# Optimization experiments

Measured on AMD Instinct MI355X. Metric: run time of the kernel, lower is better.

The kernel has to match this reference:

```python
import jax, jax.numpy as jnp
import numpy as np

DIM = 1024
H = 16
DH = 64
INNER = H * DH
SCALE = DH ** -0.5


def setup_inputs() -> dict:
    key = jax.random.key(0)
    ks = jax.random.split(key, 6)
    B, L, R = 4, 4096, 512
    x = jax.random.normal(ks[0], (B, L, DIM), dtype=jnp.float32)
    context = jax.random.normal(ks[1], (B, R, DIM), dtype=jnp.float32)
    s = DIM ** -0.5
    Wq = jax.random.normal(ks[2], (DIM, INNER), dtype=jnp.float32) * s
    Wk = jax.random.normal(ks[3], (DIM, INNER), dtype=jnp.float32) * s
    Wv = jax.random.normal(ks[4], (DIM, INNER), dtype=jnp.float32) * s
    Wo = jax.random.normal(ks[5], (INNER, DIM), dtype=jnp.float32) * (INNER ** -0.5)
    return {"x": x, "context": context, "Wq": Wq, "Wk": Wk, "Wv": Wv, "Wo": Wo}


def reference(x, context, Wq, Wk, Wv, Wo):
    B, L, _ = x.shape
    R = context.shape[1]
    # project and split heads: (B, H, L/R, Dh)
    q = (x @ Wq).reshape(B, L, H, DH).transpose(0, 2, 1, 3)
    k = (context @ Wk).reshape(B, R, H, DH).transpose(0, 2, 1, 3)
    v = (context @ Wv).reshape(B, R, H, DH).transpose(0, 2, 1, 3)
    scores = jnp.einsum('bhld,bhrd->bhlr', q, k) * SCALE  # (B,H,L,R)
    attn = jax.nn.softmax(scores, axis=-1)
    out = jnp.einsum('bhlr,bhrd->bhld', attn, v)
    out = out.transpose(0, 2, 1, 3).reshape(B, L, INNER)
    return out @ Wo
```

## Files before the change

### kernel.cpp

```cpp
#include <hip/hip_runtime.h>
#include <hip/hip_bf16.h>

#define DIMC 1024
#define HEADS 16
#define DHEAD 64
#define LQ 4096
#define RK 512
#define BATCH 4

#define QSCALE 0.18033688011112042f

using bf16x8  = __attribute__((ext_vector_type(8))) __bf16;
using short4v = __attribute__((ext_vector_type(4))) short;
using f32x4   = __attribute__((ext_vector_type(4))) float;

__device__ inline ushort f2bf(float f) {
  __hip_bfloat16 h = __float2bfloat16(f);
  return *reinterpret_cast<ushort*>(&h);
}

__device__ inline float exp2_fast(float x) {
  float r; asm("v_exp_f32 %0, %1" : "=v"(r) : "v"(x)); return r;
}

__global__ __launch_bounds__(256) void prep(const float* __restrict__ x,
    const float* __restrict__ ctx, ushort* __restrict__ xb,
    ushort* __restrict__ ctxb,
    const float* __restrict__ W0, const float* __restrict__ W1,
    const float* __restrict__ W2, const float* __restrict__ W3,
    ushort* __restrict__ D0, ushort* __restrict__ D1,
    ushort* __restrict__ D2, ushort* __restrict__ D3) {
  __shared__ ushort tile[32][33];
  const int bid = blockIdx.x;
  if (bid < 9216) {
    size_t i = ((size_t)bid * 256 + threadIdx.x) * 8;
    const float* src; ushort* dst; size_t off;
    if (i < (size_t)16777216) { src = x; dst = xb; off = i; }
    else { src = ctx; dst = ctxb; off = i - 16777216; }
    float4 a = *(const float4*)(src + off);
    float4 b = *(const float4*)(src + off + 4);
    ushort u[8];
    u[0]=f2bf(a.x); u[1]=f2bf(a.y); u[2]=f2bf(a.z); u[3]=f2bf(a.w);
    u[4]=f2bf(b.x); u[5]=f2bf(b.y); u[6]=f2bf(b.z); u[7]=f2bf(b.w);
    *(uint4*)(dst + off) = *(const uint4*)u;
    return;
  }
  const int tb = bid - 9216;
  const int z = tb >> 10, rem = tb & 1023;
  const int bx = rem & 31, by = rem >> 5;
  const float* src = (z == 0) ? W0 : (z == 1) ? W1 : (z == 2) ? W2 : W3;
  ushort* dst = (z == 0) ? D0 : (z == 1) ? D1 : (z == 2) ? D2 : D3;
  const int tx = threadIdx.x & 31, ty = threadIdx.x >> 5;
  const int xg = bx * 32 + tx;
  #pragma unroll
  for (int j = 0; j < 32; j += 8)
    tile[ty + j][tx] = f2bf(src[(size_t)(by * 32 + ty + j) * DIMC + xg]);
  __syncthreads();
  const int xo = by * 32 + tx;
  #pragma unroll
  for (int j = 0; j < 32; j += 8)
    dst[(size_t)(bx * 32 + ty + j) * DIMC + xo] = tile[tx][ty + j];
}

__global__ __launch_bounds__(256, 4) void gemm_qkv(const ushort* __restrict__ xb,
    const ushort* __restrict__ ctxb, const ushort* __restrict__ WqT,
    const ushort* __restrict__ WkvT, ushort* __restrict__ Qw,
    ushort* __restrict__ Kw, ushort* __restrict__ Vt) {
  __shared__ ushort As[128 * 64];
  __shared__ ushort Bs[128 * 64];
  const int tid  = threadIdx.x;
  const int wave = tid >> 6, lane = tid & 63;
  const int lr = lane & 15, quad = lane >> 4;
  const ushort* A; const ushort* Bt; size_t m0, n0; int seg;
  if (blockIdx.y < 128) {
    int bid = blockIdx.y * 8 + blockIdx.x;
    int swz = (bid & 7) * 128 + (bid >> 3);
    m0 = (size_t)(swz >> 3) * 128;
    n0 = (size_t)(swz & 7) * 128;
    A = xb; Bt = WqT; seg = 0;
  } else {
    int bid = (blockIdx.y - 128) * 8 + blockIdx.x;
    int swz = (bid & 7) * 32 + (bid >> 3);
    m0 = (size_t)(swz >> 4) * 128;
    n0 = (size_t)(swz & 15) * 128;
    A = ctxb; Bt = WkvT; seg = 1;
  }
  const int wm = (wave >> 1) * 64, wn = (wave & 1) * 64;
  const int rsw = lr & 7;
  f32x4 acc[4][4] = {};
  for (int k0 = 0; k0 < DIMC; k0 += 64) {
    __syncthreads();
    #pragma unroll
    for (int t = 0; t < 4; ++t) {
      int c = (wave * 4 + t) * 64 + lane;
      int row = c >> 3, cc = c & 7;
      int col = (cc ^ (row & 7)) * 8;
      const ushort* ga = A  + (m0 + row) * DIMC + k0 + col;
      const ushort* gb = Bt + (n0 + row) * DIMC + k0 + col;
      __builtin_amdgcn_global_load_lds(
          (__attribute__((address_space(1))) void*)ga,
          (__attribute__((address_space(3))) void*)(As + (size_t)(wave * 4 + t) * 512),
          16, 0, 0);
      __builtin_amdgcn_global_load_lds(
          (__attribute__((address_space(1))) void*)gb,
          (__attribute__((address_space(3))) void*)(Bs + (size_t)(wave * 4 + t) * 512),
          16, 0, 0);
    }
    __syncthreads();
    #pragma unroll
    for (int ks = 0; ks < 2; ++ks) {
      bf16x8 af[4], bfr[4];
      #pragma unroll
      for (int mt = 0; mt < 4; ++mt)
        af[mt] = *(const bf16x8*)(As + (wm + mt * 16 + lr) * 64
                                     + (((ks * 4 + quad) ^ rsw) * 8));
      #pragma unroll
      for (int nt = 0; nt < 4; ++nt)
        bfr[nt] = *(const bf16x8*)(Bs + (wn + nt * 16 + lr) * 64
                                      + (((ks * 4 + quad) ^ rsw) * 8));
      #pragma unroll
      for (int mt = 0; mt < 4; ++mt)
        #pragma unroll
        for (int nt = 0; nt < 4; ++nt)
          acc[mt][nt] = __builtin_amdgcn_mfma_f32_16x16x32_bf16(
              af[mt], bfr[nt], acc[mt][nt], 0, 0, 0);
    }
  }
  if (seg == 0) {
    #pragma unroll
    for (int mt = 0; mt < 4; ++mt)
      #pragma unroll
      for (int nt = 0; nt < 4; ++nt)
        #pragma unroll
        for (int j = 0; j < 4; ++j) {
          size_t m = m0 + wm + mt * 16 + quad * 4 + j;
          size_t n = n0 + wn + nt * 16 + lr;
          Qw[m * DIMC + n] = f2bf(acc[mt][nt][j] * QSCALE);
        }
  } else if (n0 < 1024) {
    #pragma unroll
    for (int mt = 0; mt < 4; ++mt)
      #pragma unroll
      for (int nt = 0; nt < 4; ++nt)
        #pragma unroll
        for (int j = 0; j < 4; ++j) {
          size_t m = m0 + wm + mt * 16 + quad * 4 + j;
          size_t n = n0 + wn + nt * 16 + lr;
          Kw[m * DIMC + n] = f2bf(acc[mt][nt][j]);
        }
  } else {
    #pragma unroll
    for (int mt = 0; mt < 4; ++mt)
      #pragma unroll
      for (int nt = 0; nt < 4; ++nt) {
        size_t m = m0 + wm + mt * 16 + quad * 4;
        int hcol = (int)(n0 + wn + nt * 16 + lr) - 1024;
        int h = hcol >> 6, dh = hcol & 63;
        int bb = (int)(m >> 9), r = (int)(m & 511);
        ushort o4[4];
        #pragma unroll
        for (int j = 0; j < 4; ++j) o4[j] = f2bf(acc[mt][nt][j]);
        *(ushort4*)(Vt + (((size_t)bb * HEADS + h) * 64 + dh) * RK + r) =
            *(const ushort4*)o4;
      }
  }
}

__global__ __launch_bounds__(256, 4) void gemm_bt(const ushort* __restrict__ A,
    const ushort* __restrict__ Bt, float* __restrict__ C32) {
  __shared__ ushort As[128 * 64];
  __shared__ ushort Bs[128 * 64];
  const int tid  = threadIdx.x;
  const int wave = tid >> 6, lane = tid & 63;
  const int lr = lane & 15, quad = lane >> 4;
  const int nbx = gridDim.x;
  const int bid = blockIdx.y * nbx + blockIdx.x;
  const int cpx = (nbx * gridDim.y) >> 3;
  const int swz = (bid & 7) * cpx + (bid >> 3);
  const int bx = swz % nbx, by = swz / nbx;
  const size_t m0 = (size_t)by * 128;
  const size_t n0 = (size_t)bx * 128;
  const int wm = (wave >> 1) * 64, wn = (wave & 1) * 64;
  const int rsw = lr & 7;
  f32x4 acc[4][4] = {};
  for (int k0 = 0; k0 < DIMC; k0 += 64) {
    __syncthreads();
    #pragma unroll
    for (int t = 0; t < 4; ++t) {
      int c = (wave * 4 + t) * 64 + lane;
      int row = c >> 3, cc = c & 7;
      int col = (cc ^ (row & 7)) * 8;
      const ushort* ga = A  + (m0 + row) * DIMC + k0 + col;
      const ushort* gb = Bt + (n0 + row) * DIMC + k0 + col;
      __builtin_amdgcn_global_load_lds(
          (__attribute__((address_space(1))) void*)ga,
          (__attribute__((address_space(3))) void*)(As + (size_t)(wave * 4 + t) * 512),
          16, 0, 0);
      __builtin_amdgcn_global_load_lds(
          (__attribute__((address_space(1))) void*)gb,
          (__attribute__((address_space(3))) void*)(Bs + (size_t)(wave * 4 + t) * 512),
          16, 0, 0);
    }
    __syncthreads();
    #pragma unroll
    for (int ks = 0; ks < 2; ++ks) {
      bf16x8 af[4], bfr[4];
      #pragma unroll
      for (int mt = 0; mt < 4; ++mt)
        af[mt] = *(const bf16x8*)(As + (wm + mt * 16 + lr) * 64
                                     + (((ks * 4 + quad) ^ rsw) * 8));
      #pragma unroll
      for (int nt = 0; nt < 4; ++nt)
        bfr[nt] = *(const bf16x8*)(Bs + (wn + nt * 16 + lr) * 64
                                      + (((ks * 4 + quad) ^ rsw) * 8));
      #pragma unroll
      for (int mt = 0; mt < 4; ++mt)
        #pragma unroll
        for (int nt = 0; nt < 4; ++nt)
          acc[mt][nt] = __builtin_amdgcn_mfma_f32_16x16x32_bf16(
              af[mt], bfr[nt], acc[mt][nt], 0, 0, 0);
    }
  }
  #pragma unroll
  for (int mt = 0; mt < 4; ++mt)
    #pragma unroll
    for (int nt = 0; nt < 4; ++nt)
      #pragma unroll
      for (int j = 0; j < 4; ++j) {
        size_t m = m0 + wm + mt * 16 + quad * 4 + j;
        size_t n = n0 + wn + nt * 16 + lr;
        C32[m * DIMC + n] = acc[mt][nt][j];
      }
}

__global__ __launch_bounds__(256) void attn(ushort* __restrict__ QO,
    const ushort* __restrict__ K, const ushort* __restrict__ Vt) {
  __shared__ __align__(16) ushort Ks[128 * 64];
  __shared__ __align__(16) ushort Vs[64 * 128];
  const int tid  = threadIdx.x;
  const int wave = tid >> 6, lane = tid & 63;
  const int lr = lane & 15, quad = lane >> 4;
  const int b = blockIdx.z, h = blockIdx.y, qb = blockIdx.x;
  const int lsw = (lr & 7) << 3;

  bf16x8 bq[2];
  {
    size_t row = (size_t)b * LQ + qb * 64 + wave * 16 + lr;
    const ushort* qp = QO + row * DIMC + h * DHEAD + quad * 8;
    bq[0] = *(const bf16x8*)(qp);
    bq[1] = *(const bf16x8*)(qp + 32);
  }

  const int krow = tid >> 3, kcol = (tid & 7) * 8;
  const int vrow = tid >> 4, vcol = (tid & 15) * 8;
  const int kwsw = (krow & 7) << 3;
  const int vwsw = (vrow & 7) << 3;
  const ushort* Kbase = K  + ((size_t)b * RK) * DIMC + h * DHEAD;
  const ushort* Vbase = Vt + (((size_t)b * HEADS + h) * 64) * RK;

  uint4 kr0, kr1, kr2, kr3, vr0, vr1, vr2, vr3;
#define LOADK(rc_, i_) \
  (*(const uint4*)(Kbase + (size_t)((rc_) * 128 + (i_) * 32 + krow) * DIMC + kcol))
#define LOADV(rc_, i_) \
  (*(const uint4*)(Vbase + (size_t)((i_) * 16 + vrow) * RK + (rc_) * 128 + vcol))
#define ISSUE(rc_) do {                                      \
    kr0 = LOADK(rc_, 0); kr1 = LOADK(rc_, 1);                \
    kr2 = LOADK(rc_, 2); kr3 = LOADK(rc_, 3);                \
    vr0 = LOADV(rc_, 0); vr1 = LOADV(rc_, 1);                \
    vr2 = LOADV(rc_, 2); vr3 = LOADV(rc_, 3);                \
  } while (0)

  ISSUE(0);

  float mi = -1e30f, li = 0.f;
  f32x4 o[4] = {};

  for (int rc = 0; rc < 4; ++rc) {
    __syncthreads();
    *(uint4*)(Ks + ((((0 * 32 + krow) * 64) + kcol) ^ kwsw)) = kr0;
    *(uint4*)(Ks + ((((1 * 32 + krow) * 64) + kcol) ^ kwsw)) = kr1;
    *(uint4*)(Ks + ((((2 * 32 + krow) * 64) + kcol) ^ kwsw)) = kr2;
    *(uint4*)(Ks + ((((3 * 32 + krow) * 64) + kcol) ^ kwsw)) = kr3;
    *(uint4*)(Vs + ((((0 * 16 + vrow) * 128) + vcol) ^ vwsw)) = vr0;
    *(uint4*)(Vs + ((((1 * 16 + vrow) * 128) + vcol) ^ vwsw)) = vr1;
    *(uint4*)(Vs + ((((2 * 16 + vrow) * 128) + vcol) ^ vwsw)) = vr2;
    *(uint4*)(Vs + ((((3 * 16 + vrow) * 128) + vcol) ^ vwsw)) = vr3;
    __syncthreads();
    if (rc < 3) ISSUE(rc + 1);

    float s[8][4];
    __builtin_amdgcn_s_setprio(1);
    #pragma unroll
    for (int nt = 0; nt < 8; ++nt) {
      f32x4 acc = {};
      acc = __builtin_amdgcn_mfma_f32_16x16x32_bf16(
          *(const bf16x8*)(Ks + ((((nt * 16 + lr) * 64) + quad * 8) ^ lsw)),
          bq[0], acc, 0, 0, 0);
      acc = __builtin_amdgcn_mfma_f32_16x16x32_bf16(
          *(const bf16x8*)(Ks + ((((nt * 16 + lr) * 64) + quad * 8 + 32) ^ lsw)),
          bq[1], acc, 0, 0, 0);
      #pragma unroll
      for (int j = 0; j < 4; ++j) s[nt][j] = acc[j];
    }
    __builtin_amdgcn_s_setprio(0);

    float c0 = s[0][0], c1 = s[0][1], c2 = s[0][2], c3 = s[0][3];
    #pragma unroll
    for (int nt = 1; nt < 8; ++nt) {
      c0 = fmaxf(c0, s[nt][0]); c1 = fmaxf(c1, s[nt][1]);
      c2 = fmaxf(c2, s[nt][2]); c3 = fmaxf(c3, s[nt][3]);
    }
    float cm = fmaxf(fmaxf(c0, c1), fmaxf(c2, c3));
    cm = fmaxf(cm, __shfl_xor(cm, 16));
    cm = fmaxf(cm, __shfl_xor(cm, 32));

    if (!__all(cm - mi <= 8.f)) {
      float mnew = fmaxf(mi, cm);
      float alpha = exp2_fast(mi - mnew);
      mi = mnew;
      li *= alpha;
      float a_bc[4];
      #pragma unroll
      for (int j = 0; j < 4; ++j) a_bc[j] = __shfl(alpha, quad * 4 + j, 16);
      #pragma unroll
      for (int n2 = 0; n2 < 4; ++n2)
        #pragma unroll
        for (int j = 0; j < 4; ++j) o[n2][j] *= a_bc[j];
    }

    short4v pf[8];
    float r0 = 0.f, r1 = 0.f, r2 = 0.f, r3 = 0.f;
    #pragma unroll
    for (int nt = 0; nt < 8; ++nt) {
      float p0 = exp2_fast(s[nt][0] - mi);
      float p1 = exp2_fast(s[nt][1] - mi);
      float p2 = exp2_fast(s[nt][2] - mi);
      float p3 = exp2_fast(s[nt][3] - mi);
      r0 += p0; r1 += p1; r2 += p2; r3 += p3;
      pf[nt][0] = (short)f2bf(p0); pf[nt][1] = (short)f2bf(p1);
      pf[nt][2] = (short)f2bf(p2); pf[nt][3] = (short)f2bf(p3);
    }
    float rs = (r0 + r1) + (r2 + r3);
    rs += __shfl_xor(rs, 16);
    rs += __shfl_xor(rs, 32);
    li += rs;

    __builtin_amdgcn_s_setprio(1);
    #pragma unroll
    for (int kt = 0; kt < 8; ++kt)
      #pragma unroll
      for (int n2 = 0; n2 < 4; ++n2) {
        short4v bv = *(const short4v*)(
            Vs + ((((n2 * 16 + lr) * 128) + kt * 16 + quad * 4) ^ lsw));
        o[n2] = __builtin_amdgcn_mfma_f32_16x16x16bf16_1k(pf[kt], bv, o[n2], 0, 0, 0);
      }
    __builtin_amdgcn_s_setprio(0);
  }
#undef LOADK
#undef LOADV
#undef ISSUE

  float li_bc[4];
  #pragma unroll
  for (int j = 0; j < 4; ++j) li_bc[j] = __shfl(li, quad * 4 + j, 16);
  #pragma unroll
  for (int n2 = 0; n2 < 4; ++n2)
    #pragma unroll
    for (int j = 0; j < 4; ++j) {
      size_t row = (size_t)b * LQ + qb * 64 + wave * 16 + quad * 4 + j;
      QO[row * DIMC + h * DHEAD + n2 * 16 + lr] = f2bf(o[n2][j] / li_bc[j]);
    }
}

extern "C" void kernel_launch(void* const* d_in, const int* in_sizes, int n_in,
                              void* d_out, int out_size, void* d_ws, size_t ws_size,
                              hipStream_t stream) {
  const float* x   = (const float*)d_in[0];
  const float* ctx = (const float*)d_in[1];

  ushort* outs = (ushort*)d_out;
  ushort* xb   = outs;
  ushort* ctxb = outs + (size_t)16777216;
  ushort* WqT  = outs + (size_t)18874368;
  ushort* WkT  = outs + (size_t)19922944;
  ushort* WvT  = outs + (size_t)20971520;
  ushort* Kw   = outs + (size_t)22020096;
  ushort* Vt_g = outs + (size_t)24117248;

  ushort* ws  = (ushort*)d_ws;
  ushort* Qw  = ws;
  ushort* WoT = ws + (size_t)16384 * 1024;

  prep<<<13312, 256, 0, stream>>>(x, ctx, xb, ctxb,
      (const float*)d_in[2], (const float*)d_in[3], (const float*)d_in[4],
      (const float*)d_in[5], WqT, WkT, WvT, WoT);
  gemm_qkv<<<dim3(8, 160), 256, 0, stream>>>(xb, ctxb, WqT, WkT, Qw, Kw, Vt_g);
  attn<<<dim3(LQ / 64, HEADS, BATCH), 256, 0, stream>>>(Qw, Kw, Vt_g);
  gemm_bt<<<dim3(8, 128), 256, 0, stream>>>(Qw, WoT, (float*)d_out);
}
```

Baseline: 302.2 us.

## Replace Q and output projections with 256x256 pipelined 8-wave GEMM

Splits the fused QKV launch into a separate K/V GEMM and a new 256x256-tile, 512-thread GEMM that also handles the output projection. The new kernel uses a multi-buffered LDS ring with explicit vmcnt waits, barriers and setprio, so global-to-LDS loads overlap MFMA work and operand reuse per tile goes up. The cost is larger LDS use (128 KB per block), a single block per CU, and fragile hand-tuned wait counts.

```diff
diff --git a/kernel.cpp b/kernel.cpp
--- a/kernel.cpp
+++ b/kernel.cpp
@@ -62,29 +62,18 @@
     dst[(size_t)(bx * 32 + ty + j) * DIMC + xo] = tile[tx][ty + j];
 }
 
-__global__ __launch_bounds__(256, 4) void gemm_qkv(const ushort* __restrict__ xb,
-    const ushort* __restrict__ ctxb, const ushort* __restrict__ WqT,
-    const ushort* __restrict__ WkvT, ushort* __restrict__ Qw,
-    ushort* __restrict__ Kw, ushort* __restrict__ Vt) {
+__global__ __launch_bounds__(256, 4) void gemm_kv(const ushort* __restrict__ A,
+    const ushort* __restrict__ Bt, ushort* __restrict__ Kw,
+    ushort* __restrict__ Vt) {
   __shared__ ushort As[128 * 64];
   __shared__ ushort Bs[128 * 64];
   const int tid  = threadIdx.x;
   const int wave = tid >> 6, lane = tid & 63;
   const int lr = lane & 15, quad = lane >> 4;
-  const ushort* A; const ushort* Bt; size_t m0, n0; int seg;
-  if (blockIdx.y < 128) {
-    int bid = blockIdx.y * 8 + blockIdx.x;
-    int swz = (bid & 7) * 128 + (bid >> 3);
-    m0 = (size_t)(swz >> 3) * 128;
-    n0 = (size_t)(swz & 7) * 128;
-    A = xb; Bt = WqT; seg = 0;
-  } else {
-    int bid = (blockIdx.y - 128) * 8 + blockIdx.x;
-    int swz = (bid & 7) * 32 + (bid >> 3);
-    m0 = (size_t)(swz >> 4) * 128;
-    n0 = (size_t)(swz & 15) * 128;
-    A = ctxb; Bt = WkvT; seg = 1;
-  }
+  const int bid = blockIdx.y * 16 + blockIdx.x;
+  const int swz = (bid & 7) * 32 + (bid >> 3);
+  const size_t m0 = (size_t)(swz >> 4) * 128;
+  const size_t n0 = (size_t)(swz & 15) * 128;
   const int wm = (wave >> 1) * 64, wn = (wave & 1) * 64;
   const int rsw = lr & 7;
   f32x4 acc[4][4] = {};
@@ -126,18 +115,7 @@
               af[mt], bfr[nt], acc[mt][nt], 0, 0, 0);
     }
   }
-  if (seg == 0) {
-    #pragma unroll
-    for (int mt = 0; mt < 4; ++mt)
-      #pragma unroll
-      for (int nt = 0; nt < 4; ++nt)
-        #pragma unroll
-        for (int j = 0; j < 4; ++j) {
-          size_t m = m0 + wm + mt * 16 + quad * 4 + j;
-          size_t n = n0 + wn + nt * 16 + lr;
-          Qw[m * DIMC + n] = f2bf(acc[mt][nt][j] * QSCALE);
-        }
-  } else if (n0 < 1024) {
+  if (n0 < 1024) {
     #pragma unroll
     for (int mt = 0; mt < 4; ++mt)
       #pragma unroll
@@ -166,71 +144,148 @@
   }
 }
 
-__global__ __launch_bounds__(256, 4) void gemm_bt(const ushort* __restrict__ A,
-    const ushort* __restrict__ Bt, float* __restrict__ C32) {
-  __shared__ ushort As[128 * 64];
-  __shared__ ushort Bs[128 * 64];
+__global__ __launch_bounds__(512, 2) void gemm256(const ushort* __restrict__ A,
+    const ushort* __restrict__ Bt, void* __restrict__ Cv, const int mode) {
+  __shared__ ushort As[32768];
+  __shared__ ushort Bs[32768];
   const int tid  = threadIdx.x;
   const int wave = tid >> 6, lane = tid & 63;
   const int lr = lane & 15, quad = lane >> 4;
-  const int nbx = gridDim.x;
-  const int bid = blockIdx.y * nbx + blockIdx.x;
-  const int cpx = (nbx * gridDim.y) >> 3;
-  const int swz = (bid & 7) * cpx + (bid >> 3);
-  const int bx = swz % nbx, by = swz / nbx;
-  const size_t m0 = (size_t)by * 128;
-  const size_t n0 = (size_t)bx * 128;
-  const int wm = (wave >> 1) * 64, wn = (wave & 1) * 64;
-  const int rsw = lr & 7;
-  f32x4 acc[4][4] = {};
-  for (int k0 = 0; k0 < DIMC; k0 += 64) {
-    __syncthreads();
-    #pragma unroll
-    for (int t = 0; t < 4; ++t) {
-      int c = (wave * 4 + t) * 64 + lane;
-      int row = c >> 3, cc = c & 7;
-      int col = (cc ^ (row & 7)) * 8;
-      const ushort* ga = A  + (m0 + row) * DIMC + k0 + col;
-      const ushort* gb = Bt + (n0 + row) * DIMC + k0 + col;
-      __builtin_amdgcn_global_load_lds(
-          (__attribute__((address_space(1))) void*)ga,
-          (__attribute__((address_space(3))) void*)(As + (size_t)(wave * 4 + t) * 512),
-          16, 0, 0);
-      __builtin_amdgcn_global_load_lds(
-          (__attribute__((address_space(1))) void*)gb,
-          (__attribute__((address_space(3))) void*)(Bs + (size_t)(wave * 4 + t) * 512),
-          16, 0, 0);
-    }
-    __syncthreads();
-    #pragma unroll
-    for (int ks = 0; ks < 2; ++ks) {
-      bf16x8 af[4], bfr[4];
-      #pragma unroll
-      for (int mt = 0; mt < 4; ++mt)
-        af[mt] = *(const bf16x8*)(As + (wm + mt * 16 + lr) * 64
-                                     + (((ks * 4 + quad) ^ rsw) * 8));
-      #pragma unroll
-      for (int nt = 0; nt < 4; ++nt)
-        bfr[nt] = *(const bf16x8*)(Bs + (wn + nt * 16 + lr) * 64
-                                      + (((ks * 4 + quad) ^ rsw) * 8));
-      #pragma unroll
-      for (int mt = 0; mt < 4; ++mt)
-        #pragma unroll
-        for (int nt = 0; nt < 4; ++nt)
-          acc[mt][nt] = __builtin_amdgcn_mfma_f32_16x16x32_bf16(
-              af[mt], bfr[nt], acc[mt][nt], 0, 0, 0);
-    }
-  }
-  #pragma unroll
-  for (int mt = 0; mt < 4; ++mt)
-    #pragma unroll
-    for (int nt = 0; nt < 4; ++nt)
-      #pragma unroll
-      for (int j = 0; j < 4; ++j) {
-        size_t m = m0 + wm + mt * 16 + quad * 4 + j;
-        size_t n = n0 + wn + nt * 16 + lr;
-        C32[m * DIMC + n] = acc[mt][nt][j];
-      }
+  const int bid = blockIdx.y * gridDim.x + blockIdx.x;
+  const int swz = (bid & 7) * 32 + (bid >> 3);
+  const size_t m0 = (size_t)(swz >> 2) * 256;
+  const size_t n0 = (size_t)(swz & 3) * 256;
+  const int wm = (wave >> 2) * 128, wn = (wave & 3) * 64;
+
+  const int lp   = lane ^ ((lane >> 3) & 3);
+  const int srow = wave * 32 + (lp >> 2);
+  const int skc  = (lp & 3) * 8;
+  const int ld0  = wave * 1024 + lane * 8;
+
+  const int qoff = (((quad * 16) ^ (((lr >> 1) & 3) << 4)) >> 1);
+
+#define STG_(dst_, src_, base_, t_, kh_) do {                                  \
+    const ushort* s_ = (src_) + ((size_t)((base_) + srow)) * DIMC              \
+                     + (t_) * 64 + (kh_) * 32 + skc;                           \
+    ushort* d_ = (dst_) + ((((t_) & 1) * 2 + (kh_)) * 8192) + ld0;             \
+    __builtin_amdgcn_global_load_lds(                                          \
+        (__attribute__((address_space(1))) void*)s_,                           \
+        (__attribute__((address_space(3))) void*)d_, 16, 0, 0);                \
+    __builtin_amdgcn_global_load_lds(                                          \
+        (__attribute__((address_space(1))) void*)(s_ + (size_t)16 * DIMC),     \
+        (__attribute__((address_space(3))) void*)(d_ + 512), 16, 0, 0);        \
+  } while (0)
+
+#define RDB4_(t_, kh_)                                                         \
+    bfr[0] = *(const bf16x8*)(Bs + (((t_)&1)*2 + (kh_))*8192 + (wn +  0 + lr)*32 + qoff); \
+    bfr[1] = *(const bf16x8*)(Bs + (((t_)&1)*2 + (kh_))*8192 + (wn + 16 + lr)*32 + qoff); \
+    bfr[2] = *(const bf16x8*)(Bs + (((t_)&1)*2 + (kh_))*8192 + (wn + 32 + lr)*32 + qoff); \
+    bfr[3] = *(const bf16x8*)(Bs + (((t_)&1)*2 + (kh_))*8192 + (wn + 48 + lr)*32 + qoff)
+
+#define RDA4_(mb_, t_, kh_)                                                    \
+    a0_ = *(const bf16x8*)(As + (((t_)&1)*2 + (kh_))*8192 + (wm + ((mb_)+0)*16 + lr)*32 + qoff); \
+    a1_ = *(const bf16x8*)(As + (((t_)&1)*2 + (kh_))*8192 + (wm + ((mb_)+1)*16 + lr)*32 + qoff); \
+    a2_ = *(const bf16x8*)(As + (((t_)&1)*2 + (kh_))*8192 + (wm + ((mb_)+2)*16 + lr)*32 + qoff); \
+    a3_ = *(const bf16x8*)(As + (((t_)&1)*2 + (kh_))*8192 + (wm + ((mb_)+3)*16 + lr)*32 + qoff)
+
+#define MF16_(mb_)                                                             \
+    acc[(mb_)+0][0] = __builtin_amdgcn_mfma_f32_16x16x32_bf16(a0_, bfr[0], acc[(mb_)+0][0], 0,0,0); \
+    acc[(mb_)+1][0] = __builtin_amdgcn_mfma_f32_16x16x32_bf16(a1_, bfr[0], acc[(mb_)+1][0], 0,0,0); \
+    acc[(mb_)+2][0] = __builtin_amdgcn_mfma_f32_16x16x32_bf16(a2_, bfr[0], acc[(mb_)+2][0], 0,0,0); \
+    acc[(mb_)+3][0] = __builtin_amdgcn_mfma_f32_16x16x32_bf16(a3_, bfr[0], acc[(mb_)+3][0], 0,0,0); \
+    acc[(mb_)+0][1] = __builtin_amdgcn_mfma_f32_16x16x32_bf16(a0_, bfr[1], acc[(mb_)+0][1], 0,0,0); \
+    acc[(mb_)+1][1] = __builtin_amdgcn_mfma_f32_16x16x32_bf16(a1_, bfr[1], acc[(mb_)+1][1], 0,0,0); \
+    acc[(mb_)+2][1] = __builtin_amdgcn_mfma_f32_16x16x32_bf16(a2_, bfr[1], acc[(mb_)+2][1], 0,0,0); \
+    acc[(mb_)+3][1] = __builtin_amdgcn_mfma_f32_16x16x32_bf16(a3_, bfr[1], acc[(mb_)+3][1], 0,0,0); \
+    acc[(mb_)+0][2] = __builtin_amdgcn_mfma_f32_16x16x32_bf16(a0_, bfr[2], acc[(mb_)+0][2], 0,0,0); \
+    acc[(mb_)+1][2] = __builtin_amdgcn_mfma_f32_16x16x32_bf16(a1_, bfr[2], acc[(mb_)+1][2], 0,0,0); \
+    acc[(mb_)+2][2] = __builtin_amdgcn_mfma_f32_16x16x32_bf16(a2_, bfr[2], acc[(mb_)+2][2], 0,0,0); \
+    acc[(mb_)+3][2] = __builtin_amdgcn_mfma_f32_16x16x32_bf16(a3_, bfr[2], acc[(mb_)+3][2], 0,0,0); \
+    acc[(mb_)+0][3] = __builtin_amdgcn_mfma_f32_16x16x32_bf16(a0_, bfr[3], acc[(mb_)+0][3], 0,0,0); \
+    acc[(mb_)+1][3] = __builtin_amdgcn_mfma_f32_16x16x32_bf16(a1_, bfr[3], acc[(mb_)+1][3], 0,0,0); \
+    acc[(mb_)+2][3] = __builtin_amdgcn_mfma_f32_16x16x32_bf16(a2_, bfr[3], acc[(mb_)+2][3], 0,0,0); \
+    acc[(mb_)+3][3] = __builtin_amdgcn_mfma_f32_16x16x32_bf16(a3_, bfr[3], acc[(mb_)+3][3], 0,0,0)
+
+#define VMW8 asm volatile("s_waitcnt vmcnt(8)" ::: "memory")
+#define VMW4 asm volatile("s_waitcnt vmcnt(4)" ::: "memory")
+#define VMW0 asm volatile("s_waitcnt vmcnt(0)" ::: "memory")
+#define VMNONE ((void)0)
+
+#define PHASE_(t_, kh_, mb_, RDB_, TAILVM_, ...) do {                          \
+    if (RDB_) { RDB4_(t_, kh_); }                                              \
+    bf16x8 a0_, a1_, a2_, a3_;                                                 \
+    RDA4_(mb_, t_, kh_);                                                       \
+    __VA_ARGS__;                                                               \
+    __builtin_amdgcn_s_barrier();                                              \
+    asm volatile("s_waitcnt lgkmcnt(0)" ::: "memory");                         \
+    __builtin_amdgcn_sched_barrier(0);                                         \
+    __builtin_amdgcn_s_setprio(1);                                             \
+    MF16_(mb_);                                                                \
+    __builtin_amdgcn_s_setprio(0);                                             \
+    TAILVM_;                                                                   \
+    __builtin_amdgcn_s_barrier();                                              \
+  } while (0)
+
+  bf16x8 bfr[4];
+  f32x4 acc[8][4] = {};
+
+  STG_(As, A,  m0, 0, 0); STG_(Bs, Bt, n0, 0, 0);
+  STG_(As, A,  m0, 0, 1); STG_(Bs, Bt, n0, 0, 1);
+  STG_(As, A,  m0, 1, 0); STG_(Bs, Bt, n0, 1, 0);
+  VMW8;
+  __builtin_amdgcn_s_barrier();
+
+  for (int I = 0; I < 7; ++I) {
+    const int t = 2 * I;
+    PHASE_(t,     0, 0, 1, VMNONE, STG_(As, A,  m0, t + 1, 1));
+    PHASE_(t,     0, 4, 0, VMW8,   STG_(Bs, Bt, n0, t + 1, 1));
+    PHASE_(t,     1, 0, 1, VMNONE, STG_(As, A,  m0, t + 2, 0));
+    PHASE_(t,     1, 4, 0, VMW8,   STG_(Bs, Bt, n0, t + 2, 0));
+    PHASE_(t + 1, 0, 0, 1, VMNONE, STG_(As, A,  m0, t + 2, 1));
+    PHASE_(t + 1, 0, 4, 0, VMW8,   STG_(Bs, Bt, n0, t + 2, 1));
+    PHASE_(t + 1, 1, 0, 1, VMNONE, STG_(As, A,  m0, t + 3, 0));
+    PHASE_(t + 1, 1, 4, 0, VMW8,   STG_(Bs, Bt, n0, t + 3, 0));
+  }
+  PHASE_(14, 0, 0, 1, VMNONE, STG_(As, A,  m0, 15, 1));
+  PHASE_(14, 0, 4, 0, VMW8,   STG_(Bs, Bt, n0, 15, 1));
+  PHASE_(14, 1, 0, 1, VMNONE, VMNONE);
+  PHASE_(14, 1, 4, 0, VMW4,   VMNONE);
+  PHASE_(15, 0, 0, 1, VMNONE, VMNONE);
+  PHASE_(15, 0, 4, 0, VMW0,   VMNONE);
+  PHASE_(15, 1, 0, 1, VMNONE, VMNONE);
+  PHASE_(15, 1, 4, 0, VMNONE, VMNONE);
+
+#undef STG_
+#undef RDB4_
+#undef RDA4_
+#undef MF16_
+#undef PHASE_
+
+  if (mode == 0) {
+    ushort* C16 = (ushort*)Cv;
+    #pragma unroll
+    for (int mf = 0; mf < 8; ++mf)
+      #pragma unroll
+      for (int nf = 0; nf < 4; ++nf)
+        #pragma unroll
+        for (int j = 0; j < 4; ++j) {
+          size_t m = m0 + wm + mf * 16 + quad * 4 + j;
+          size_t n = n0 + wn + nf * 16 + lr;
+          C16[m * DIMC + n] = f2bf(acc[mf][nf][j] * QSCALE);
+        }
+  } else {
+    float* C32 = (float*)Cv;
+    #pragma unroll
+    for (int mf = 0; mf < 8; ++mf)
+      #pragma unroll
+      for (int nf = 0; nf < 4; ++nf)
+        #pragma unroll
+        for (int j = 0; j < 4; ++j) {
+          size_t m = m0 + wm + mf * 16 + quad * 4 + j;
+          size_t n = n0 + wn + nf * 16 + lr;
+          C32[m * DIMC + n] = acc[mf][nf][j];
+        }
+  }
 }
 
 __global__ __launch_bounds__(256) void attn(ushort* __restrict__ QO,
@@ -394,7 +449,8 @@
   prep<<<13312, 256, 0, stream>>>(x, ctx, xb, ctxb,
       (const float*)d_in[2], (const float*)d_in[3], (const float*)d_in[4],
       (const float*)d_in[5], WqT, WkT, WvT, WoT);
-  gemm_qkv<<<dim3(8, 160), 256, 0, stream>>>(xb, ctxb, WqT, WkT, Qw, Kw, Vt_g);
+  gemm_kv<<<dim3(16, 16), 256, 0, stream>>>(ctxb, WkT, Kw, Vt_g);
+  gemm256<<<dim3(4, 64), 512, 0, stream>>>(xb, WqT, Qw, 0);
   attn<<<dim3(LQ / 64, HEADS, BATCH), 256, 0, stream>>>(Qw, Kw, Vt_g);
-  gemm_bt<<<dim3(8, 128), 256, 0, stream>>>(Qw, WoT, (float*)d_out);
-}
+  gemm256<<<dim3(4, 64), 512, 0, stream>>>(Qw, WoT, (float*)d_out, 1);
+}
```

After: 307.3 us. Within noise of the previous version (+1.7%).
